# Optimization experiments

Hardware: AMD Instinct MI355X
Metric: run time of the kernel (lower is better)

Reference implementation:

```python
import jax, jax.numpy as jnp
import numpy as np

ALPHA, BETA, GAMMA, DELTA, EPSILON = 1.0, 0.15, 0.05, 0.0, 0.1
C1 = (0.01 * 255.0) ** 2
C2 = (0.03 * 255.0) ** 2


def _gaussian_kernel11():
    # cv2.getGaussianKernel(11, 1.5) outer product
    g = np.exp(-((np.arange(11) - 5.0) ** 2) / (2.0 * 1.5 ** 2))
    g = g / g.sum()
    return jnp.asarray(np.outer(g, g), dtype=jnp.float32)


def _to_uint8_float(x):
    # clamp to [-1,1], map to [0,1], scale to 255, uint8 truncation (floor)
    x = jnp.clip(x, -1.0, 1.0)
    x01 = jnp.clip((x + 1.0) * 0.5, 0.0, 1.0)
    return jnp.floor(jnp.clip(x01 * 255.0, 0.0, 255.0))


def _depthwise_valid_conv(x, kern2d):
    # x: [B,C,H,W]; 11x11 gaussian, VALID padding == filter2D + [5:-5,5:-5] crop
    C = x.shape[1]
    k = jnp.broadcast_to(kern2d[None, None], (C, 1, 11, 11))
    return jax.lax.conv_general_dilated(
        x, k, window_strides=(1, 1), padding='VALID',
        dimension_numbers=('NCHW', 'OIHW', 'NCHW'), feature_group_count=C)


def _ssim_per_image(img1, img2):
    # img1/img2: [B,C,H,W] floats in [0,255]; basicsr-style SSIM per channel, mean over C
    kern = _gaussian_kernel11()
    conv = lambda t: _depthwise_valid_conv(t, kern)
    mu1, mu2 = conv(img1), conv(img2)
    mu1_sq, mu2_sq, mu1_mu2 = mu1 * mu1, mu2 * mu2, mu1 * mu2
    sigma1_sq = conv(img1 * img1) - mu1_sq
    sigma2_sq = conv(img2 * img2) - mu2_sq
    sigma12 = conv(img1 * img2) - mu1_mu2
    ssim_map = ((2.0 * mu1_mu2 + C1) * (2.0 * sigma12 + C2)) / (
        (mu1_sq + mu2_sq + C1) * (sigma1_sq + sigma2_sq + C2))
    return jnp.mean(ssim_map, axis=(1, 2, 3))  # [B]


def _psnr_per_image(img1, img2):
    mse = jnp.mean((img1 - img2) ** 2, axis=(1, 2, 3))
    psnr = 10.0 * jnp.log10((255.0 ** 2) / jnp.maximum(mse, 1e-12))
    return jnp.where(mse == 0.0, 100.0, psnr)


def setup_inputs() -> dict:
    key = jax.random.key(0)
    k1, k2 = jax.random.split(key)
    shape = (4, 1, 2048, 2048)
    pred = jax.random.normal(k1, shape, dtype=jnp.float32) * 0.5
    target = jax.random.normal(k2, shape, dtype=jnp.float32) * 0.5
    return {"pred": pred, "target": target}


def reference(pred, target):
    # L1 loss
    l1 = jnp.mean(jnp.abs(pred - target))

    # edge-aware gradient loss (finite differences along H and W)
    gx = lambda t: t[:, :, :-1, :] - t[:, :, 1:, :]
    gy = lambda t: t[:, :, :, :-1] - t[:, :, :, 1:]
    grad_loss = (jnp.mean(jnp.abs(gx(pred) - gx(target))) +
                 jnp.mean(jnp.abs(gy(pred) - gy(target))))

    # physical consistency: per-image/channel mean & unbiased std stats + range penalty
    pm = jnp.mean(pred, axis=(2, 3))
    tm = jnp.mean(target, axis=(2, 3))
    energy = jnp.mean((pm - tm) ** 2)
    n = pred.shape[2] * pred.shape[3]
    ps = jnp.sqrt(jnp.sum((pred - pm[:, :, None, None]) ** 2, axis=(2, 3)) / (n - 1))
    ts = jnp.sqrt(jnp.sum((target - tm[:, :, None, None]) ** 2, axis=(2, 3)) / (n - 1))
    dist = jnp.mean((ps - ts) ** 2)
    range_pen = jnp.mean(jax.nn.relu(jnp.abs(pred) - 1.0))
    phys = energy + 0.5 * dist + 0.1 * range_pen

    # SSIM / PSNR on uint8-quantized [0,255] images (metric path, no gradient)
    p8 = _to_uint8_float(pred)
    t8 = _to_uint8_float(target)
    ssim_mean = jnp.clip(jnp.mean(_ssim_per_image(p8, t8)), 0.0, 1.0)
    psnr_mean = jnp.mean(_psnr_per_image(p8, t8))
    ssim_loss = 1.0 - ssim_mean

    total = (ALPHA * l1 + BETA * grad_loss + GAMMA * phys +
             EPSILON * jax.lax.stop_gradient(ssim_loss))
    return total, psnr_mean, ssim_mean
```

## Files before the change

### kernel.cpp

```cpp
#include <hip/hip_runtime.h>
#include <math.h>

#define HDIM 2048
#define WDIM 2048
#define NPIX (HDIM*WDIM)
#define OUTW 2038

#define C1F 6.5025f
#define C2F 58.5225f

constexpr int TH   = 64, TW = 32;
constexpr int IN_R = 80;
constexpr int IQ_S = 72;
constexpr int IQ_H = IN_R * IQ_S;
constexpr int HT_R = 80;
constexpr int HT_A = 32 * HT_R;
constexpr int NBLK = 8192;

struct GaussW { float g[11]; };

typedef _Float16 half8 __attribute__((ext_vector_type(8)));
typedef float    f32x4 __attribute__((ext_vector_type(4)));
typedef float    f32x2 __attribute__((ext_vector_type(2)));

__device__ __forceinline__ float quant_u8f(float x) {
    float c = __builtin_amdgcn_fmed3f(x, -1.0f, 1.0f);
    return truncf((c + 1.0f) * 127.5f);
}

__device__ __forceinline__ f32x2 quant2(f32x2 x) {
    f32x2 c = { __builtin_amdgcn_fmed3f(x.x, -1.0f, 1.0f),
                __builtin_amdgcn_fmed3f(x.y, -1.0f, 1.0f) };
    f32x2 v = (c + 1.0f) * 127.5f;
    return { truncf(v.x), truncf(v.y) };
}

__device__ __forceinline__ unsigned pk2(float a, float b) {
    return __builtin_bit_cast(unsigned, __builtin_amdgcn_cvt_pkrtz(a, b));
}

__global__ __launch_bounds__(256, 5) void amsr2_fused(
        const float* __restrict__ pred, const float* __restrict__ targ,
        float* __restrict__ pr, GaussW gw)
{
    __shared__ alignas(16) _Float16 Ubuf[5 * HT_A];
    __shared__ float sred[16][10];
    _Float16* Iq = Ubuf;
    _Float16* Tg = Ubuf + 2 * IQ_H;

    const int b  = blockIdx.z;
    const int r0 = blockIdx.y * TH;
    const int c0 = blockIdx.x * TW;
    const float* pb = pred + (size_t)b * NPIX;
    const float* tb = targ + (size_t)b * NPIX;
    const bool interior = (blockIdx.y < 31) && (blockIdx.x < 63);

    if (threadIdx.x < 16) {
        int n = threadIdx.x;
#pragma unroll
        for (int i = 0; i < 16; ++i) ((unsigned*)Tg)[n * 16 + i] = 0u;
#pragma unroll
        for (int j = 0; j < 11; ++j) Tg[n * 32 + n + j] = (_Float16)gw.g[j];
    }

    float s0 = 0.f, s1 = 0.f, s2 = 0.f, s3 = 0.f, ssum = 0.f;
    f32x2 s4v = {0.f, 0.f}, s5v = {0.f, 0.f}, s6v = {0.f, 0.f},
          s7v = {0.f, 0.f}, s8v = {0.f, 0.f}, ssv = {0.f, 0.f};

    if (interior) {
        float4 cA[2], cB[2], cAD[2], cBD[2];
        float cp5[2], ct5[2];
#pragma unroll
        for (int i = 0; i < 2; ++i) {
            int item = threadIdx.x + i * 256;
            int r = item >> 3, d = item & 7;
            const float* prow = pb + (size_t)(r0 + r) * WDIM + (c0 + d * 4);
            const float* trow = tb + (size_t)(r0 + r) * WDIM + (c0 + d * 4);
            cA[i]  = *(const float4*)prow;
            cB[i]  = *(const float4*)trow;
            cAD[i] = *(const float4*)(prow + WDIM);
            cBD[i] = *(const float4*)(trow + WDIM);
            cp5[i] = prow[4];
            ct5[i] = trow[4];
        }
        float4 h0A, h0B, h1A, h1B;
        const int h0r = threadIdx.x >> 2, h0d = 8 + (threadIdx.x & 3);
        {
            const float* prow = pb + (size_t)(r0 + h0r) * WDIM + (c0 + h0d * 4);
            const float* trow = tb + (size_t)(r0 + h0r) * WDIM + (c0 + h0d * 4);
            h0A = *(const float4*)prow;
            h0B = *(const float4*)trow;
        }
        const bool act1 = threadIdx.x < 192;
        const int rq1 = threadIdx.x / 12;
        const int h1r = 64 + rq1, h1d = threadIdx.x - rq1 * 12;
        if (act1) {
            const float* prow = pb + (size_t)(r0 + h1r) * WDIM + (c0 + h1d * 4);
            const float* trow = tb + (size_t)(r0 + h1r) * WDIM + (c0 + h1d * 4);
            h1A = *(const float4*)prow;
            h1B = *(const float4*)trow;
        }

#pragma unroll
        for (int i = 0; i < 2; ++i) {
            int item = threadIdx.x + i * 256;
            int r = item >> 3, d = item & 7;
            float4 a4 = cA[i], b4 = cB[i], ad = cAD[i], bd = cBD[i];
            float p5 = cp5[i], t5 = ct5[i];

            f32x2 a01 = {a4.x, a4.y}, a23 = {a4.z, a4.w};
            f32x2 b01 = {b4.x, b4.y}, b23 = {b4.z, b4.w};
            f32x2 dd01 = a01 - b01, dd23 = a23 - b23;
            float dd4 = p5 - t5;
            f32x2 g01 = f32x2{ad.x, ad.y} - f32x2{bd.x, bd.y};
            f32x2 g23 = f32x2{ad.z, ad.w} - f32x2{bd.z, bd.w};

            s0 += fabsf(dd01.x); s0 += fabsf(dd01.y);
            s0 += fabsf(dd23.x); s0 += fabsf(dd23.y);
            s1 += fabsf(dd01.x - g01.x); s1 += fabsf(dd01.y - g01.y);
            s1 += fabsf(dd23.x - g23.x); s1 += fabsf(dd23.y - g23.y);
            s2 += fabsf(dd01.x - dd01.y); s2 += fabsf(dd01.y - dd23.x);
            s2 += fabsf(dd23.x - dd23.y); s2 += fabsf(dd23.y - dd4);
            s3 += fmaxf(fabsf(a4.x) - 1.0f, 0.0f);
            s3 += fmaxf(fabsf(a4.y) - 1.0f, 0.0f);
            s3 += fmaxf(fabsf(a4.z) - 1.0f, 0.0f);
            s3 += fmaxf(fabsf(a4.w) - 1.0f, 0.0f);
            s4v += a01; s4v += a23;
            s5v += b01; s5v += b23;
            s6v += a01 * a01; s6v += a23 * a23;
            s7v += b01 * b01; s7v += b23 * b23;
            f32x2 qp01 = quant2(a01), qp23 = quant2(a23);
            f32x2 qt01 = quant2(b01), qt23 = quant2(b23);
            f32x2 qd01 = qp01 - qt01, qd23 = qp23 - qt23;
            s8v += qd01 * qd01; s8v += qd23 * qd23;

            *(uint2*)&Iq[r * IQ_S + d * 4] =
                make_uint2(pk2(qp01.x, qp01.y), pk2(qp23.x, qp23.y));
            *(uint2*)&Iq[IQ_H + r * IQ_S + d * 4] =
                make_uint2(pk2(qt01.x, qt01.y), pk2(qt23.x, qt23.y));
        }
        {
            f32x2 qp01 = quant2(f32x2{h0A.x, h0A.y}), qp23 = quant2(f32x2{h0A.z, h0A.w});
            f32x2 qt01 = quant2(f32x2{h0B.x, h0B.y}), qt23 = quant2(f32x2{h0B.z, h0B.w});
            *(uint2*)&Iq[h0r * IQ_S + h0d * 4] =
                make_uint2(pk2(qp01.x, qp01.y), pk2(qp23.x, qp23.y));
            *(uint2*)&Iq[IQ_H + h0r * IQ_S + h0d * 4] =
                make_uint2(pk2(qt01.x, qt01.y), pk2(qt23.x, qt23.y));
        }
        if (act1) {
            f32x2 qp01 = quant2(f32x2{h1A.x, h1A.y}), qp23 = quant2(f32x2{h1A.z, h1A.w});
            f32x2 qt01 = quant2(f32x2{h1B.x, h1B.y}), qt23 = quant2(f32x2{h1B.z, h1B.w});
            *(uint2*)&Iq[h1r * IQ_S + h1d * 4] =
                make_uint2(pk2(qp01.x, qp01.y), pk2(qp23.x, qp23.y));
            *(uint2*)&Iq[IQ_H + h1r * IQ_S + h1d * 4] =
                make_uint2(pk2(qt01.x, qt01.y), pk2(qt23.x, qt23.y));
        }
    } else {
#pragma unroll
        for (int i = 0; i < 2; ++i) {
            int item = threadIdx.x + i * 256;
            int r = item >> 3, d = item & 7;
            int gr = r0 + r, gc = c0 + d * 4;
            const float* prow = pb + (size_t)gr * WDIM + gc;
            const float* trow = tb + (size_t)gr * WDIM + gc;
            float4 a4 = *(const float4*)prow;
            float4 b4 = *(const float4*)trow;
            bool down = gr < (HDIM - 1);
            bool hasR = (gc + 4) < WDIM;
            float4 z4 = make_float4(0.f, 0.f, 0.f, 0.f);
            float4 ad = down ? *(const float4*)(prow + WDIM) : z4;
            float4 bd = down ? *(const float4*)(trow + WDIM) : z4;
            float p5 = hasR ? prow[4] : 0.0f;
            float t5 = hasR ? trow[4] : 0.0f;
            float pv[4] = {a4.x, a4.y, a4.z, a4.w};
            float tv[4] = {b4.x, b4.y, b4.z, b4.w};
            float pd[4] = {ad.x, ad.y, ad.z, ad.w};
            float td[4] = {bd.x, bd.y, bd.z, bd.w};
            float qp[4], qt[4];
#pragma unroll
            for (int k = 0; k < 4; ++k) { qp[k] = quant_u8f(pv[k]); qt[k] = quant_u8f(tv[k]); }
#pragma unroll
            for (int k = 0; k < 4; ++k) {
                float av = pv[k], bv = tv[k];
                float dd = av - bv;
                s0 += fabsf(dd);
                s3 += fmaxf(fabsf(av) - 1.0f, 0.0f);
                s4v.x += av;  s5v.x += bv;
                s6v.x = fmaf(av, av, s6v.x);
                s7v.x = fmaf(bv, bv, s7v.x);
                if (down) s1 += fabsf(dd - (pd[k] - td[k]));
                float nr  = (k < 3) ? pv[k + 1] : p5;
                float nt2 = (k < 3) ? tv[k + 1] : t5;
                if (k < 3 || hasR) s2 += fabsf(dd - (nr - nt2));
                float qd = qp[k] - qt[k];
                s8v.x = fmaf(qd, qd, s8v.x);
            }
            *(uint2*)&Iq[r * IQ_S + d * 4] =
                make_uint2(pk2(qp[0], qp[1]), pk2(qp[2], qp[3]));
            *(uint2*)&Iq[IQ_H + r * IQ_S + d * 4] =
                make_uint2(pk2(qt[0], qt[1]), pk2(qt[2], qt[3]));
        }
#pragma unroll
        for (int ph = 0; ph < 2; ++ph) {
            int r, d;
            bool active = true;
            if (ph == 0) { int h = threadIdx.x; r = h >> 2; d = 8 + (h & 3); }
            else {
                int h = threadIdx.x;
                active = h < 192;
                int rq = h / 12;
                r = 64 + rq; d = h - rq * 12;
            }
            if (active) {
                int gr = r0 + r, gc = c0 + d * 4;
                bool rowok = gr < HDIM;
                const float* prow = pb + (size_t)gr * WDIM + gc;
                const float* trow = tb + (size_t)gr * WDIM + gc;
                float qp[4], qt[4];
                if (rowok && (gc + 3) < WDIM) {
                    float4 a4 = *(const float4*)prow;
                    float4 b4 = *(const float4*)trow;
                    qp[0]=quant_u8f(a4.x); qp[1]=quant_u8f(a4.y); qp[2]=quant_u8f(a4.z); qp[3]=quant_u8f(a4.w);
                    qt[0]=quant_u8f(b4.x); qt[1]=quant_u8f(b4.y); qt[2]=quant_u8f(b4.z); qt[3]=quant_u8f(b4.w);
                } else {
#pragma unroll
                    for (int k = 0; k < 4; ++k) {
                        bool ok = rowok && (gc + k) < WDIM;
                        qp[k] = ok ? quant_u8f(prow[k]) : 0.0f;
                        qt[k] = ok ? quant_u8f(trow[k]) : 0.0f;
                    }
                }
                *(uint2*)&Iq[r * IQ_S + d * 4] =
                    make_uint2(pk2(qp[0], qp[1]), pk2(qp[2], qp[3]));
                *(uint2*)&Iq[IQ_H + r * IQ_S + d * 4] =
                    make_uint2(pk2(qt[0], qt[1]), pk2(qt[2], qt[3]));
            }
        }
    }
    __syncthreads();

    const int lane = threadIdx.x & 63;
    const int wid  = threadIdx.x >> 6;
    const int q    = lane >> 4;
    const int ml   = lane & 15;
    const half8 gfrag = *(const half8*)&Tg[ml * 32 + q * 8];
    const f32x4 zero4 = {0.f, 0.f, 0.f, 0.f};

    const int npos = (wid < 2) ? 3 : 2;
    half8 hap[3], hat[3];
#pragma unroll
    for (int i = 0; i < 3; ++i) {
        if (i < npos) {
            int pos = wid + i * 4;
            int rb = (pos >> 1) * 16;
            int cb = pos & 1;
            int base = (rb + ml) * IQ_S + cb * 16 + q * 8;
            hap[i] = *(const half8*)&Iq[base];
            hat[i] = *(const half8*)&Iq[IQ_H + base];
        }
    }
    __syncthreads();

#pragma unroll
    for (int i = 0; i < 3; ++i) {
        if (i < npos) {
            int pos = wid + i * 4;
            int rb = (pos >> 1) * 16;
            int cb = pos & 1;
            const half8 ap = hap[i];
            const half8 at = hat[i];
            f32x4 d0 = __builtin_amdgcn_mfma_f32_16x16x32_f16(ap,      gfrag, zero4, 0, 0, 0);
            f32x4 d1 = __builtin_amdgcn_mfma_f32_16x16x32_f16(at,      gfrag, zero4, 0, 0, 0);
            f32x4 d2 = __builtin_amdgcn_mfma_f32_16x16x32_f16(ap * ap, gfrag, zero4, 0, 0, 0);
            f32x4 d3 = __builtin_amdgcn_mfma_f32_16x16x32_f16(at * at, gfrag, zero4, 0, 0, 0);
            f32x4 d4 = __builtin_amdgcn_mfma_f32_16x16x32_f16(ap * at, gfrag, zero4, 0, 0, 0);
            int hb = (cb * 16 + ml) * HT_R + rb + q * 4;
            *(uint2*)&Ubuf[0 * HT_A + hb] = make_uint2(pk2(d0[0], d0[1]), pk2(d0[2], d0[3]));
            *(uint2*)&Ubuf[1 * HT_A + hb] = make_uint2(pk2(d1[0], d1[1]), pk2(d1[2], d1[3]));
            *(uint2*)&Ubuf[2 * HT_A + hb] = make_uint2(pk2(d2[0], d2[1]), pk2(d2[2], d2[3]));
            *(uint2*)&Ubuf[3 * HT_A + hb] = make_uint2(pk2(d3[0], d3[1]), pk2(d3[2], d3[3]));
            *(uint2*)&Ubuf[4 * HT_A + hb] = make_uint2(pk2(d4[0], d4[1]), pk2(d4[2], d4[3]));
        }
    }
    __syncthreads();

    const int th_ = min(TH, OUTW - r0);
    const int tw_ = min(TW, OUTW - c0);
    for (int vp = wid; vp < 8; vp += 4) {
        int rb2 = (vp >> 1) * 16;
        int cb2 = vp & 1;
        f32x4 acc[5];
#pragma unroll
        for (int arr = 0; arr < 5; ++arr) {
            const half8 bf = *(const half8*)&Ubuf[arr * HT_A +
                                                  (cb2 * 16 + ml) * HT_R + rb2 + q * 8];
            acc[arr] = __builtin_amdgcn_mfma_f32_16x16x32_f16(gfrag, bf, zero4, 0, 0, 0);
        }
        if (interior) {
#pragma unroll
            for (int pp = 0; pp < 2; ++pp) {
                f32x2 mu1 = {acc[0][2*pp], acc[0][2*pp+1]};
                f32x2 mu2 = {acc[1][2*pp], acc[1][2*pp+1]};
                f32x2 vpp = {acc[2][2*pp], acc[2][2*pp+1]};
                f32x2 vtt = {acc[3][2*pp], acc[3][2*pp+1]};
                f32x2 vpt = {acc[4][2*pp], acc[4][2*pp+1]};
                f32x2 mu12 = mu1 * mu2, mu1s = mu1 * mu1, mu2s = mu2 * mu2;
                f32x2 sg12 = vpt - mu12, sg1 = vpp - mu1s, sg2 = vtt - mu2s;
                f32x2 num = (2.0f * mu12 + C1F) * (2.0f * sg12 + C2F);
                f32x2 den = (mu1s + mu2s + C1F) * (sg1 + sg2 + C2F);
                f32x2 rp = { __builtin_amdgcn_rcpf(den.x),
                             __builtin_amdgcn_rcpf(den.y) };
                ssv += num * rp;
            }
        } else {
            int col = cb2 * 16 + ml;
#pragma unroll
            for (int reg = 0; reg < 4; ++reg) {
                int row = rb2 + q * 4 + reg;
                if (row < th_ && col < tw_) {
                    float mu1 = acc[0][reg], mu2 = acc[1][reg];
                    float vpp = acc[2][reg], vtt = acc[3][reg], vpt = acc[4][reg];
                    float mu1s = mu1 * mu1, mu2s = mu2 * mu2, mu12 = mu1 * mu2;
                    float sg1 = vpp - mu1s, sg2 = vtt - mu2s, sg12 = vpt - mu12;
                    float num = (2.0f * mu12 + C1F) * (2.0f * sg12 + C2F);
                    float den = (mu1s + mu2s + C1F) * (sg1 + sg2 + C2F);
                    ssum += num * __builtin_amdgcn_rcpf(den);
                }
            }
        }
    }

    float st10[10];
    st10[0] = s0; st10[1] = s1; st10[2] = s2; st10[3] = s3;
    st10[4] = s4v.x + s4v.y; st10[5] = s5v.x + s5v.y;
    st10[6] = s6v.x + s6v.y; st10[7] = s7v.x + s7v.y;
    st10[8] = s8v.x + s8v.y; st10[9] = ssum + ssv.x + ssv.y;
#pragma unroll
    for (int c = 0; c < 10; ++c) {
        float v = st10[c];
        v += __shfl_xor(v, 8);
        v += __shfl_xor(v, 4);
        v += __shfl_xor(v, 2);
        v += __shfl_xor(v, 1);
        st10[c] = v;
    }
    if ((lane & 15) == 0) {
        int g = wid * 4 + (lane >> 4);
#pragma unroll
        for (int c = 0; c < 10; ++c) sred[g][c] = st10[c];
    }
    __syncthreads();
    if (threadIdx.x < 10) {
        int c = threadIdx.x;
        float t = 0.0f;
#pragma unroll
        for (int g = 0; g < 16; ++g) t += sred[g][c];
        int bid = ((b * 32) + blockIdx.y) * 64 + blockIdx.x;
        pr[c * NBLK + bid] = t;
    }
}

__global__ __launch_bounds__(256) void amsr2_final(
        const float* __restrict__ pr, float* __restrict__ out)
{
    __shared__ double seg[40];
    int wid = threadIdx.x >> 6, lane = threadIdx.x & 63;
    for (int sidx = wid; sidx < 40; sidx += 4) {
        int c = sidx >> 2, b = sidx & 3;
        const float* base = pr + c * NBLK + b * 2048;
        float4 v[8];
#pragma unroll
        for (int it = 0; it < 8; ++it)
            v[it] = *(const float4*)(base + (it * 64 + lane) * 4);
        double acc = 0.0;
#pragma unroll
        for (int it = 0; it < 8; ++it)
            acc += (double)v[it].x + (double)v[it].y + (double)v[it].z + (double)v[it].w;
        for (int off = 32; off > 0; off >>= 1) acc += __shfl_down(acc, off);
        if (lane == 0) seg[sidx] = acc;
    }
    __syncthreads();
    if (threadIdx.x != 0) return;
    const double n = (double)NPIX;
    double sum0 = 0, sum1 = 0, sum2 = 0, sum3 = 0;
    for (int b = 0; b < 4; ++b) {
        sum0 += seg[0*4+b]; sum1 += seg[1*4+b]; sum2 += seg[2*4+b]; sum3 += seg[3*4+b];
    }
    double l1   = sum0 / (4.0 * n);
    double grad = sum1 / (4.0 * 2047.0 * 2048.0) + sum2 / (4.0 * 2048.0 * 2047.0);
    double energy = 0.0, dist = 0.0, psnr_sum = 0.0, ssim_sum = 0.0;
    for (int b = 0; b < 4; ++b) {
        double Sp  = seg[4*4+b],  St  = seg[5*4+b];
        double Spp = seg[6*4+b],  Stt = seg[7*4+b];
        double Su8 = seg[8*4+b],  Sss = seg[9*4+b];
        double pm = Sp / n, tm = St / n;
        double dm = pm - tm; energy += dm * dm;
        double vp = (Spp - n * pm * pm) / (n - 1.0);
        double vt = (Stt - n * tm * tm) / (n - 1.0);
        double ps = sqrt(fmax(vp, 0.0)), ts = sqrt(fmax(vt, 0.0));
        double dd = ps - ts; dist += dd * dd;
        double mse = Su8 / n;
        double psnr = (mse == 0.0) ? 100.0 : 10.0 * log10(65025.0 / fmax(mse, 1e-12));
        psnr_sum += psnr;
        ssim_sum += Sss / ((double)OUTW * (double)OUTW);
    }
    energy *= 0.25; dist *= 0.25;
    double range_pen = sum3 / (4.0 * n);
    double phys = energy + 0.5 * dist + 0.1 * range_pen;
    double ssim_mean = fmin(fmax(ssim_sum * 0.25, 0.0), 1.0);
    double total = l1 + 0.15 * grad + 0.05 * phys + 0.1 * (1.0 - ssim_mean);
    out[0] = (float)total;
    out[1] = (float)(psnr_sum * 0.25);
    out[2] = (float)ssim_mean;
}

extern "C" void kernel_launch(void* const* d_in, const int* in_sizes, int n_in,
                              void* d_out, int out_size, void* d_ws, size_t ws_size,
                              hipStream_t stream)
{
    (void)in_sizes; (void)n_in; (void)out_size; (void)ws_size;
    const float* pred = (const float*)d_in[0];
    const float* targ = (const float*)d_in[1];
    float* out = (float*)d_out;
    float* pr  = (float*)d_ws;

    GaussW gw;
    {
        double e[11], sm = 0.0;
        for (int i = 0; i < 11; ++i) {
            double d = (double)(i - 5);
            e[i] = exp(-(d * d) / 4.5);
            sm += e[i];
        }
        for (int i = 0; i < 11; ++i) gw.g[i] = (float)(e[i] / sm);
    }

    amsr2_fused<<<dim3(64, 32, 4), 256, 0, stream>>>(pred, targ, pr, gw);
    amsr2_final<<<1, 256, 0, stream>>>(pr, out);
}
```

Baseline: 174.4 us.

## Merge p² and t² convolution channels into one pre-scaled sum channel

The SSIM denominator only needs sigma1²+sigma2², so conv(p²) and conv(t²) are folded into a single conv of (p²+t²)/4, computed in fp16 and rescaled by 4 afterward. This drops one of five MFMA channels in both separable passes and shrinks the shared intermediate buffer. The quantized input row stride is also narrowed, occupancy hint changed from 5 to 4, and a scheduling barrier added after global loads. The fp16 sum with the 0.25 scale risks precision loss (values up to about 32512 stay within fp16 range).

```diff
diff --git a/kernel.cpp b/kernel.cpp
--- a/kernel.cpp
+++ b/kernel.cpp
@@ -11,10 +11,11 @@
 
 constexpr int TH   = 64, TW = 32;
 constexpr int IN_R = 80;
-constexpr int IQ_S = 72;
+constexpr int IQ_S = 56;
 constexpr int IQ_H = IN_R * IQ_S;
 constexpr int HT_R = 80;
 constexpr int HT_A = 32 * HT_R;
+constexpr int NCH  = 4;
 constexpr int NBLK = 8192;
 
 struct GaussW { float g[11]; };
@@ -27,23 +28,21 @@
     float c = __builtin_amdgcn_fmed3f(x, -1.0f, 1.0f);
     return truncf((c + 1.0f) * 127.5f);
 }
-
 __device__ __forceinline__ f32x2 quant2(f32x2 x) {
     f32x2 c = { __builtin_amdgcn_fmed3f(x.x, -1.0f, 1.0f),
                 __builtin_amdgcn_fmed3f(x.y, -1.0f, 1.0f) };
     f32x2 v = (c + 1.0f) * 127.5f;
     return { truncf(v.x), truncf(v.y) };
 }
-
 __device__ __forceinline__ unsigned pk2(float a, float b) {
     return __builtin_bit_cast(unsigned, __builtin_amdgcn_cvt_pkrtz(a, b));
 }
 
-__global__ __launch_bounds__(256, 5) void amsr2_fused(
+__global__ __launch_bounds__(256, 4) void amsr2_fused(
         const float* __restrict__ pred, const float* __restrict__ targ,
         float* __restrict__ pr, GaussW gw)
 {
-    __shared__ alignas(16) _Float16 Ubuf[5 * HT_A];
+    __shared__ alignas(16) _Float16 Ubuf[NCH * HT_A];
     __shared__ float sred[16][10];
     _Float16* Iq = Ubuf;
     _Float16* Tg = Ubuf + 2 * IQ_H;
@@ -64,8 +63,7 @@
     }
 
     float s0 = 0.f, s1 = 0.f, s2 = 0.f, s3 = 0.f, ssum = 0.f;
-    f32x2 s4v = {0.f, 0.f}, s5v = {0.f, 0.f}, s6v = {0.f, 0.f},
-          s7v = {0.f, 0.f}, s8v = {0.f, 0.f}, ssv = {0.f, 0.f};
+    f32x2 s4v = {0,0}, s5v = {0,0}, s6v = {0,0}, s7v = {0,0}, s8v = {0,0}, ssv = {0,0};
 
     if (interior) {
         float4 cA[2], cB[2], cAD[2], cBD[2];
@@ -83,7 +81,7 @@
             cp5[i] = prow[4];
             ct5[i] = trow[4];
         }
-        float4 h0A, h0B, h1A, h1B;
+        float4 h0A, h0B;
         const int h0r = threadIdx.x >> 2, h0d = 8 + (threadIdx.x & 3);
         {
             const float* prow = pb + (size_t)(r0 + h0r) * WDIM + (c0 + h0d * 4);
@@ -91,6 +89,8 @@
             h0A = *(const float4*)prow;
             h0B = *(const float4*)trow;
         }
+        float4 h1A = make_float4(0.f, 0.f, 0.f, 0.f);
+        float4 h1B = h1A;
         const bool act1 = threadIdx.x < 192;
         const int rq1 = threadIdx.x / 12;
         const int h1r = 64 + rq1, h1d = threadIdx.x - rq1 * 12;
@@ -100,6 +100,7 @@
             h1A = *(const float4*)prow;
             h1B = *(const float4*)trow;
         }
+        __builtin_amdgcn_sched_barrier(0);
 
 #pragma unroll
         for (int i = 0; i < 2; ++i) {
@@ -245,6 +246,7 @@
     const int ml   = lane & 15;
     const half8 gfrag = *(const half8*)&Tg[ml * 32 + q * 8];
     const f32x4 zero4 = {0.f, 0.f, 0.f, 0.f};
+    const _Float16 hquart = (_Float16)0.25f;
 
     const int npos = (wid < 2) ? 3 : 2;
     half8 hap[3], hat[3];
@@ -269,17 +271,17 @@
             int cb = pos & 1;
             const half8 ap = hap[i];
             const half8 at = hat[i];
+            half8 m2 = (ap * hquart) * ap;
+            m2 = (at * hquart) * at + m2;
             f32x4 d0 = __builtin_amdgcn_mfma_f32_16x16x32_f16(ap,      gfrag, zero4, 0, 0, 0);
             f32x4 d1 = __builtin_amdgcn_mfma_f32_16x16x32_f16(at,      gfrag, zero4, 0, 0, 0);
-            f32x4 d2 = __builtin_amdgcn_mfma_f32_16x16x32_f16(ap * ap, gfrag, zero4, 0, 0, 0);
-            f32x4 d3 = __builtin_amdgcn_mfma_f32_16x16x32_f16(at * at, gfrag, zero4, 0, 0, 0);
-            f32x4 d4 = __builtin_amdgcn_mfma_f32_16x16x32_f16(ap * at, gfrag, zero4, 0, 0, 0);
+            f32x4 d2 = __builtin_amdgcn_mfma_f32_16x16x32_f16(m2,      gfrag, zero4, 0, 0, 0);
+            f32x4 d3 = __builtin_amdgcn_mfma_f32_16x16x32_f16(ap * at, gfrag, zero4, 0, 0, 0);
             int hb = (cb * 16 + ml) * HT_R + rb + q * 4;
             *(uint2*)&Ubuf[0 * HT_A + hb] = make_uint2(pk2(d0[0], d0[1]), pk2(d0[2], d0[3]));
             *(uint2*)&Ubuf[1 * HT_A + hb] = make_uint2(pk2(d1[0], d1[1]), pk2(d1[2], d1[3]));
             *(uint2*)&Ubuf[2 * HT_A + hb] = make_uint2(pk2(d2[0], d2[1]), pk2(d2[2], d2[3]));
             *(uint2*)&Ubuf[3 * HT_A + hb] = make_uint2(pk2(d3[0], d3[1]), pk2(d3[2], d3[3]));
-            *(uint2*)&Ubuf[4 * HT_A + hb] = make_uint2(pk2(d4[0], d4[1]), pk2(d4[2], d4[3]));
         }
     }
     __syncthreads();
@@ -289,9 +291,9 @@
     for (int vp = wid; vp < 8; vp += 4) {
         int rb2 = (vp >> 1) * 16;
         int cb2 = vp & 1;
-        f32x4 acc[5];
-#pragma unroll
-        for (int arr = 0; arr < 5; ++arr) {
+        f32x4 acc[NCH];
+#pragma unroll
+        for (int arr = 0; arr < NCH; ++arr) {
             const half8 bf = *(const half8*)&Ubuf[arr * HT_A +
                                                   (cb2 * 16 + ml) * HT_R + rb2 + q * 8];
             acc[arr] = __builtin_amdgcn_mfma_f32_16x16x32_f16(gfrag, bf, zero4, 0, 0, 0);
@@ -301,13 +303,13 @@
             for (int pp = 0; pp < 2; ++pp) {
                 f32x2 mu1 = {acc[0][2*pp], acc[0][2*pp+1]};
                 f32x2 mu2 = {acc[1][2*pp], acc[1][2*pp+1]};
-                f32x2 vpp = {acc[2][2*pp], acc[2][2*pp+1]};
-                f32x2 vtt = {acc[3][2*pp], acc[3][2*pp+1]};
-                f32x2 vpt = {acc[4][2*pp], acc[4][2*pp+1]};
+                f32x2 h2  = {acc[2][2*pp], acc[2][2*pp+1]};
+                f32x2 h12 = {acc[3][2*pp], acc[3][2*pp+1]};
                 f32x2 mu12 = mu1 * mu2, mu1s = mu1 * mu1, mu2s = mu2 * mu2;
-                f32x2 sg12 = vpt - mu12, sg1 = vpp - mu1s, sg2 = vtt - mu2s;
+                f32x2 sg12 = h12 - mu12;
+                f32x2 sgs  = 4.0f * h2 - mu1s - mu2s;
                 f32x2 num = (2.0f * mu12 + C1F) * (2.0f * sg12 + C2F);
-                f32x2 den = (mu1s + mu2s + C1F) * (sg1 + sg2 + C2F);
+                f32x2 den = (mu1s + mu2s + C1F) * (sgs + C2F);
                 f32x2 rp = { __builtin_amdgcn_rcpf(den.x),
                              __builtin_amdgcn_rcpf(den.y) };
                 ssv += num * rp;
@@ -319,11 +321,12 @@
                 int row = rb2 + q * 4 + reg;
                 if (row < th_ && col < tw_) {
                     float mu1 = acc[0][reg], mu2 = acc[1][reg];
-                    float vpp = acc[2][reg], vtt = acc[3][reg], vpt = acc[4][reg];
+                    float h2  = acc[2][reg], h12 = acc[3][reg];
                     float mu1s = mu1 * mu1, mu2s = mu2 * mu2, mu12 = mu1 * mu2;
-                    float sg1 = vpp - mu1s, sg2 = vtt - mu2s, sg12 = vpt - mu12;
+                    float sg12 = h12 - mu12;
+                    float sgs  = 4.0f * h2 - mu1s - mu2s;
                     float num = (2.0f * mu12 + C1F) * (2.0f * sg12 + C2F);
-                    float den = (mu1s + mu2s + C1F) * (sg1 + sg2 + C2F);
+                    float den = (mu1s + mu2s + C1F) * (sgs + C2F);
                     ssum += num * __builtin_amdgcn_rcpf(den);
                 }
             }
```

After: 175.0 us. No clear change (+0.3%).
